# Optimization experiments

Measured on AMD Instinct MI355X. Metric: run time of the kernel, lower is better.

## Reference

```python
import jax, jax.numpy as jnp
import numpy as np

EPSILON = 0.0014  # ODIN perturbation magnitude (init kwarg)


def _penultimate(x, W, b):
    # Simple feature extractor standing in for model.penultimate_forward:
    # flatten image and apply ReLU(linear). feat: [B, D]
    B = x.shape[0]
    return jax.nn.relu(x.reshape(B, -1) @ W + b)


def _mahalanobis_scores(feat, mu, invsig):
    # diff: [B, C, D]; y[b,c] = -diff[b,c] @ invsig @ diff[b,c]
    # Fused as a single einsum instead of the naive [B,C,D,D] broadcast.
    diff = feat[:, None, :] - mu[None, :, :]
    return -jnp.einsum('bcd,de,bce->bc', diff, invsig, diff)


def setup_inputs() -> dict:
    key = jax.random.key(0)
    k1, k2, k3, k4, k5 = jax.random.split(key, 5)
    B, C, D, IN = 1024, 100, 512, 3 * 32 * 32
    x = jax.random.uniform(k1, (B, 3, 32, 32), dtype=jnp.float32)
    W = jax.random.normal(k2, (IN, D), dtype=jnp.float32) * (1.0 / np.sqrt(IN))
    b = jax.random.normal(k3, (D,), dtype=jnp.float32) * 0.01
    mu = jax.random.normal(k4, (C, D), dtype=jnp.float32)
    # symmetric positive-definite inverse covariance
    A = jax.random.normal(k5, (D, D), dtype=jnp.float32) * (1.0 / np.sqrt(D))
    invsig = A @ A.T + jnp.eye(D, dtype=jnp.float32)
    return {"x": x, "W": W, "b": b, "mu": mu, "invsig": invsig}


def reference(x, W, b, mu, invsig):
    # FGSM step: perturb x toward increasing the max class score.
    def fgsm_loss(xx):
        y = _mahalanobis_scores(_penultimate(xx, W, b), mu, invsig)
        return jnp.max(y, axis=1).sum()

    g = jax.grad(fgsm_loss)(x)
    # torch.autograd.grad(create_graph=False) detaches the grad -> stop_gradient
    x_adv = jnp.clip(x + EPSILON * jax.lax.stop_gradient(g), 0.0, 1.0)
    # Main pass on the perturbed input.
    return _mahalanobis_scores(_penultimate(x_adv, W, b), mu, invsig)
```

## Files before the change

kernel.cpp:

```cpp
#include <hip/hip_runtime.h>
#include <hip/hip_bf16.h>

#define EPS_ODIN 0.0014f

constexpr int Bb  = 1024;
constexpr int Cc  = 100;
constexpr int Dd  = 512;
constexpr int INn = 3072;
constexpr int PITCH = 68;

using s16x8 = __attribute__((ext_vector_type(8))) short;
using s16x4 = __attribute__((ext_vector_type(4))) short;
using f32x4 = __attribute__((ext_vector_type(4))) float;

__device__ __forceinline__ short f2bf(float f) {
    __hip_bfloat16 h = __float2bfloat16(f);
    return *reinterpret_cast<short*>(&h);
}

__global__ __launch_bounds__(256) void prep_kernel(
    const float* __restrict__ x, const float* __restrict__ W,
    const float* __restrict__ invsig, const float* __restrict__ mu,
    short* __restrict__ x_b, short* __restrict__ Wt_b,
    short* __restrict__ is_b, short* __restrict__ mu_b)
{
    __shared__ float tp[32][33];
    const int tid = threadIdx.x, bid = blockIdx.x;
    const long gstride = (long)gridDim.x * 256;
    auto cvt4 = [&](const float* in, short* ob, long q) {
        long idx = q * 4;
        f32x4 v = *(const f32x4*)(in + idx);
        s16x4 o;
        #pragma unroll
        for (int j = 0; j < 4; ++j) o[j] = f2bf(v[j]);
        *(s16x4*)(ob + idx) = o;
    };
    for (long i = (long)bid * 256 + tid; i < (long)Bb * INn / 4; i += gstride) cvt4(x, x_b, i);
    for (long i = (long)bid * 256 + tid; i < (long)Dd * Dd / 4; i += gstride) cvt4(invsig, is_b, i);
    for (long i = (long)bid * 256 + tid; i < (long)112 * Dd / 4; i += gstride) {
        long idx = i * 4;
        if ((idx >> 9) < Cc) cvt4(mu, mu_b, i);
        else *(s16x4*)(mu_b + idx) = s16x4{0, 0, 0, 0};
    }

    const int tx = tid & 31, ty = tid >> 5;
    for (int tix = bid; tix < (INn / 32) * (Dd / 32); tix += gridDim.x) {
        int r0 = (tix >> 4) * 32, c0 = (tix & 15) * 32;
        #pragma unroll
        for (int i2 = 0; i2 < 4; ++i2)
            tp[ty + i2 * 8][tx] = W[(long)(r0 + ty + i2 * 8) * Dd + c0 + tx];
        __syncthreads();
        #pragma unroll
        for (int i2 = 0; i2 < 4; ++i2) {
            int c = c0 + ty + i2 * 8;
            Wt_b[(long)c * INn + r0 + tx] = f2bf(tp[tx][ty + i2 * 8]);
        }
        __syncthreads();
    }
}

__global__ __launch_bounds__(256) void im_q_kernel(
    const float* __restrict__ mu, const float* __restrict__ invsig,
    float* __restrict__ im, float* __restrict__ q)
{
    __shared__ float muc[512];
    __shared__ float red[4];
    const int tid = threadIdx.x, c = blockIdx.x;
    for (int e = tid; e < 512; e += 256) muc[e] = mu[(long)c * 512 + e];
    __syncthreads();
    const int d0 = tid, d1 = tid + 256;
    float a0 = 0.f, a1 = 0.f, a2 = 0.f, a3 = 0.f;
    for (int e = 0; e < 512; e += 2) {
        float m0 = muc[e], m1 = muc[e + 1];
        a0 = fmaf(m0, invsig[(long)e * 512 + d0], a0);
        a1 = fmaf(m0, invsig[(long)e * 512 + d1], a1);
        a2 = fmaf(m1, invsig[(long)(e + 1) * 512 + d0], a2);
        a3 = fmaf(m1, invsig[(long)(e + 1) * 512 + d1], a3);
    }
    float r0 = a0 + a2, r1 = a1 + a3;
    im[(long)c * 512 + d0] = r0;
    im[(long)c * 512 + d1] = r1;
    float s = muc[d0] * r0 + muc[d1] * r1;
    #pragma unroll
    for (int off = 32; off; off >>= 1) s += __shfl_down(s, off);
    if ((tid & 63) == 0) red[tid >> 6] = s;
    __syncthreads();
    if (tid == 0) q[c] = red[0] + red[1] + red[2] + red[3];
}

template<int EPI>
__global__ __launch_bounds__(256, 4) void gemm_b1(
    const short* __restrict__ A, const short* __restrict__ Bm,
    float* __restrict__ Cm, long K, int kcount, int N, long sstr,
    const float* __restrict__ aux1, const float* __restrict__ aux2,
    short* __restrict__ obf, float esc)
{
    __shared__ short As[128 * PITCH];
    __shared__ short Bs[64 * PITCH];
    const int tid = threadIdx.x;
    const int m0 = blockIdx.y * 128, n0 = blockIdx.x * 64;
    const long kbeg = (long)blockIdx.z * kcount;
    const int lane = tid & 63, w = tid >> 6, wm = w * 32;
    const int lrow = lane & 15, kseg = lane >> 4;
    const int srow = tid >> 3, skc = (tid & 7) * 8;
    const int nkt = kcount >> 6;

    f32x4 acc[2][4];
    #pragma unroll
    for (int i = 0; i < 2; ++i)
        #pragma unroll
        for (int j = 0; j < 4; ++j)
            acc[i][j] = f32x4{0.f, 0.f, 0.f, 0.f};

    s16x8 rA[4], rB[2];
    auto ldA = [&](int kt) {
        #pragma unroll
        for (int i = 0; i < 4; ++i)
            rA[i] = *(const s16x8*)(A + (long)(m0 + srow + i * 32) * K + kbeg + (long)kt * 64 + skc);
    };
    auto ldB = [&](int kt) {
        #pragma unroll
        for (int i = 0; i < 2; ++i)
            rB[i] = *(const s16x8*)(Bm + (long)(n0 + srow + i * 32) * K + kbeg + (long)kt * 64 + skc);
    };

    ldA(0); ldB(0);
    for (int kt = 0; kt < nkt; ++kt) {
        #pragma unroll
        for (int i = 0; i < 4; ++i)
            *(s16x8*)&As[(srow + i * 32) * PITCH + skc] = rA[i];
        #pragma unroll
        for (int i = 0; i < 2; ++i)
            *(s16x8*)&Bs[(srow + i * 32) * PITCH + skc] = rB[i];
        __syncthreads();
        if (kt + 1 < nkt) { ldA(kt + 1); ldB(kt + 1); }
        #pragma unroll
        for (int kk = 0; kk < 2; ++kk) {
            s16x8 ah[2], bfr[4];
            #pragma unroll
            for (int i = 0; i < 2; ++i)
                ah[i] = *(const s16x8*)&As[(wm + i * 16 + lrow) * PITCH + kk * 32 + kseg * 8];
            #pragma unroll
            for (int j = 0; j < 4; ++j)
                bfr[j] = *(const s16x8*)&Bs[(j * 16 + lrow) * PITCH + kk * 32 + kseg * 8];
            #pragma unroll
            for (int i = 0; i < 2; ++i)
                #pragma unroll
                for (int j = 0; j < 4; ++j)
                    acc[i][j] = __builtin_amdgcn_mfma_f32_16x16x32_bf16(ah[i], bfr[j], acc[i][j], 0, 0, 0);
        }
        __syncthreads();
    }

    const int crow = (lane >> 4) * 4, ccol = lane & 15;
    #pragma unroll
    for (int i = 0; i < 2; ++i)
        #pragma unroll
        for (int j = 0; j < 4; ++j)
            #pragma unroll
            for (int r = 0; r < 4; ++r) {
                int gm = m0 + wm + i * 16 + crow + r;
                int gn = n0 + j * 16 + ccol;
                float v = acc[i][j][r];
                if (EPI == 0) {
                    (Cm + (long)blockIdx.z * sstr)[(long)gm * 512 + gn] = v;
                } else if (EPI == 1) {
                    long cidx = (long)gm * N + gn;
                    Cm[cidx] = v;
                    obf[cidx] = f2bf(v);
                } else {
                    long cidx = (long)gm * N + gn;
                    float u = fmaxf(aux1[cidx] + aux2[gn] + esc * v, 0.f);
                    Cm[cidx] = u;
                    obf[cidx] = f2bf(u);
                }
            }
}

__global__ __launch_bounds__(256) void reduce_feat(
    const float* __restrict__ part, const float* __restrict__ bias,
    float* __restrict__ featpre, float* __restrict__ feat, short* __restrict__ fb)
{
    long idx = ((long)blockIdx.x * 256 + threadIdx.x) * 4;
    f32x4 v = *(const f32x4*)(part + idx);
    #pragma unroll
    for (int z = 1; z < 8; ++z)
        v += *(const f32x4*)(part + (long)z * Bb * Dd + idx);
    *(f32x4*)(featpre + idx) = v;
    f32x4 bb = *(const f32x4*)(bias + (idx & 511));
    s16x4 o;
    #pragma unroll
    for (int j = 0; j < 4; ++j) {
        v[j] = fmaxf(v[j] + bb[j], 0.f);
        o[j] = f2bf(v[j]);
    }
    *(f32x4*)(feat + idx) = v;
    *(s16x4*)(fb + idx) = o;
}

__global__ __launch_bounds__(256) void reduce_wtw(
    const float* __restrict__ wpart, short* __restrict__ wtw_b)
{
    long idx = ((long)blockIdx.x * 256 + threadIdx.x) * 4;
    f32x4 v = *(const f32x4*)(wpart + idx);
    #pragma unroll
    for (int z = 1; z < 8; ++z)
        v += *(const f32x4*)(wpart + (long)z * Dd * Dd + idx);
    s16x4 o;
    #pragma unroll
    for (int j = 0; j < 4; ++j) o[j] = f2bf(v[j]);
    *(s16x4*)(wtw_b + idx) = o;
}

__global__ __launch_bounds__(256) void tail_a(
    const short* __restrict__ h_b, const short* __restrict__ mu_b,
    const float* __restrict__ feat, const float* __restrict__ hbuf,
    const float* __restrict__ im, const float* __restrict__ q,
    short* __restrict__ dz_b)
{
    __shared__ f32x4 red[4][7][64];
    __shared__ int cstv[16];
    const int tid = threadIdx.x, lane = tid & 63, w = tid >> 6;
    const int m0 = blockIdx.x * 16;
    const int arow = lane & 15, kseg = lane >> 4;

    f32x4 acc[7];
    #pragma unroll
    for (int j = 0; j < 7; ++j) acc[j] = f32x4{0.f, 0.f, 0.f, 0.f};

    const long abase = (long)(m0 + arow) * 512 + w * 128 + kseg * 8;
    const long bbase = (long)arow * 512 + w * 128 + kseg * 8;
    #pragma unroll
    for (int kt = 0; kt < 4; ++kt) {
        s16x8 av = *(const s16x8*)(h_b + abase + kt * 32);
        #pragma unroll
        for (int j = 0; j < 7; ++j) {
            s16x8 bv = *(const s16x8*)(mu_b + bbase + (long)j * 16 * 512 + kt * 32);
            acc[j] = __builtin_amdgcn_mfma_f32_16x16x32_bf16(av, bv, acc[j], 0, 0, 0);
        }
    }
    #pragma unroll
    for (int j = 0; j < 7; ++j) red[w][j][lane] = acc[j];
    __syncthreads();

    if (w == 0) {
        #pragma unroll
        for (int j = 0; j < 7; ++j) {
            f32x4 s0 = red[0][j][lane];
            #pragma unroll
            for (int ww = 1; ww < 4; ++ww) s0 += red[ww][j][lane];
            acc[j] = s0;
        }
        const int crow = (lane >> 4) * 4, ccol = lane & 15;
        #pragma unroll
        for (int r = 0; r < 4; ++r) {
            float best = -INFINITY; int bestc = 0;
            #pragma unroll
            for (int j = 0; j < 7; ++j) {
                int n = j * 16 + ccol;
                if (n < 100) {
                    float v = 2.f * acc[j][r] - q[n];
                    if (v > best) { best = v; bestc = n; }
                }
            }
            #pragma unroll
            for (int mk = 1; mk <= 8; mk <<= 1) {
                float ov = __shfl_xor(best, mk);
                int   oc = __shfl_xor(bestc, mk);
                if (ov > best || (ov == best && oc < bestc)) { best = ov; bestc = oc; }
            }
            if (ccol == 0) cstv[crow + r] = bestc;
        }
    }
    __syncthreads();

    #pragma unroll
    for (int it = 0; it < 8; ++it) {
        int i4 = it * 256 + tid;
        int r = i4 >> 7, d4 = (i4 & 127) * 4;
        long gi = (long)(m0 + r) * 512 + d4;
        f32x4 fv = *(const f32x4*)(feat + gi);
        f32x4 hv = *(const f32x4*)(hbuf + gi);
        f32x4 iv = *(const f32x4*)(im + (long)cstv[r] * 512 + d4);
        s16x4 o;
        #pragma unroll
        for (int jj = 0; jj < 4; ++jj) {
            float v = (fv[jj] > 0.f) ? -2.f * (hv[jj] - iv[jj]) : 0.f;
            o[jj] = f2bf(v);
        }
        *(s16x4*)(dz_b + gi) = o;
    }
}

__global__ __launch_bounds__(256) void tail_b(
    const short* __restrict__ h_b, const short* __restrict__ mu_b,
    const float* __restrict__ feat, const float* __restrict__ hbuf,
    const float* __restrict__ q, float* __restrict__ out)
{
    __shared__ f32x4 red[4][7][64];
    __shared__ float srow[16];
    const int tid = threadIdx.x, lane = tid & 63, w = tid >> 6;
    const int m0 = blockIdx.x * 16;
    const int arow = lane & 15, kseg = lane >> 4;

    #pragma unroll
    for (int rr = 0; rr < 4; ++rr) {
        int r = w * 4 + rr;
        long gi = (long)(m0 + r) * 512 + lane * 8;
        f32x4 a0 = *(const f32x4*)(feat + gi);
        f32x4 a1 = *(const f32x4*)(feat + gi + 4);
        f32x4 b0 = *(const f32x4*)(hbuf + gi);
        f32x4 b1 = *(const f32x4*)(hbuf + gi + 4);
        float ss = 0.f;
        #pragma unroll
        for (int jj = 0; jj < 4; ++jj) ss += a0[jj] * b0[jj] + a1[jj] * b1[jj];
        #pragma unroll
        for (int off = 32; off; off >>= 1) ss += __shfl_down(ss, off);
        if (lane == 0) srow[r] = ss;
    }

    f32x4 acc[7];
    #pragma unroll
    for (int j = 0; j < 7; ++j) acc[j] = f32x4{0.f, 0.f, 0.f, 0.f};
    const long abase = (long)(m0 + arow) * 512 + w * 128 + kseg * 8;
    const long bbase = (long)arow * 512 + w * 128 + kseg * 8;
    #pragma unroll
    for (int kt = 0; kt < 4; ++kt) {
        s16x8 av = *(const s16x8*)(h_b + abase + kt * 32);
        #pragma unroll
        for (int j = 0; j < 7; ++j) {
            s16x8 bv = *(const s16x8*)(mu_b + bbase + (long)j * 16 * 512 + kt * 32);
            acc[j] = __builtin_amdgcn_mfma_f32_16x16x32_bf16(av, bv, acc[j], 0, 0, 0);
        }
    }
    #pragma unroll
    for (int j = 0; j < 7; ++j) red[w][j][lane] = acc[j];
    __syncthreads();

    if (w == 0) {
        const int crow = (lane >> 4) * 4, ccol = lane & 15;
        #pragma unroll
        for (int j = 0; j < 7; ++j) {
            int n = j * 16 + ccol;
            if (n >= 100) continue;
            f32x4 s0 = red[0][j][lane];
            #pragma unroll
            for (int ww = 1; ww < 4; ++ww) s0 += red[ww][j][lane];
            float qn = q[n];
            #pragma unroll
            for (int r = 0; r < 4; ++r)
                out[(long)(m0 + crow + r) * 100 + n] = 2.f * s0[r] - srow[crow + r] - qn;
        }
    }
}

extern "C" void kernel_launch(void* const* d_in, const int* in_sizes, int n_in,
                              void* d_out, int out_size, void* d_ws, size_t ws_size,
                              hipStream_t stream)
{
    const float* x      = (const float*)d_in[0];
    const float* W      = (const float*)d_in[1];
    const float* bias   = (const float*)d_in[2];
    const float* mu     = (const float*)d_in[3];
    const float* invsig = (const float*)d_in[4];
    float* out = (float*)d_out;

    char* wp = (char*)d_ws;
    auto alloc = [&](size_t bytes) { char* p = wp; wp += (bytes + 255) & ~size_t(255); return p; };
    short* x_b   = (short*)alloc((size_t)Bb * INn * 2);
    short* Wt_b  = (short*)alloc((size_t)Dd * INn * 2);
    short* is_b  = (short*)alloc((size_t)Dd * Dd * 2);
    short* mu_b  = (short*)alloc((size_t)112 * Dd * 2);
    short* wtw_b = (short*)alloc((size_t)Dd * Dd * 2);
    float* im    = (float*)alloc((size_t)Cc * Dd * 4);
    float* q     = (float*)alloc(512);
    float* part  = (float*)alloc((size_t)8 * Bb * Dd * 4);
    float* wpart = (float*)alloc((size_t)8 * Dd * Dd * 4);
    float* featpre = (float*)alloc((size_t)Bb * Dd * 4);
    float* feat  = (float*)alloc((size_t)Bb * Dd * 4);
    short* f_b   = (short*)alloc((size_t)Bb * Dd * 2);
    float* hbuf  = (float*)alloc((size_t)Bb * Dd * 4);
    short* h_b   = (short*)alloc((size_t)Bb * Dd * 2);
    short* dz_b  = (short*)alloc((size_t)Bb * Dd * 2);

    dim3 blk(256);

    prep_kernel<<<512, blk, 0, stream>>>(x, W, invsig, mu, x_b, Wt_b, is_b, mu_b);
    im_q_kernel<<<Cc, blk, 0, stream>>>(mu, invsig, im, q);
    gemm_b1<0><<<dim3(8, 4, 8), blk, 0, stream>>>(
        Wt_b, Wt_b, wpart, INn, INn / 8, Dd, (long)Dd * Dd, nullptr, nullptr, nullptr, 0.f);
    reduce_wtw<<<256, blk, 0, stream>>>(wpart, wtw_b);
    gemm_b1<0><<<dim3(8, 8, 8), blk, 0, stream>>>(
        x_b, Wt_b, part, INn, INn / 8, Dd, (long)Bb * Dd, nullptr, nullptr, nullptr, 0.f);
    reduce_feat<<<512, blk, 0, stream>>>(part, bias, featpre, feat, f_b);
    gemm_b1<1><<<dim3(8, 8), blk, 0, stream>>>(
        f_b, is_b, hbuf, Dd, Dd, Dd, 0, nullptr, nullptr, h_b, 0.f);
    tail_a<<<Bb / 16, blk, 0, stream>>>(h_b, mu_b, feat, hbuf, im, q, dz_b);
    gemm_b1<3><<<dim3(8, 8), blk, 0, stream>>>(
        dz_b, wtw_b, feat, Dd, Dd, Dd, 0, featpre, bias, f_b, EPS_ODIN);
    gemm_b1<1><<<dim3(8, 8), blk, 0, stream>>>(
        f_b, is_b, hbuf, Dd, Dd, Dd, 0, nullptr, nullptr, h_b, 0.f);
    tail_b<<<Bb / 16, blk, 0, stream>>>(h_b, mu_b, feat, hbuf, q, out);
}
```

Before: 108.8 us.

## Convert x to bf16 inside GEMM, exploit WtW symmetry, use smaller square-GEMM tiles

Removes the separate fp32-to-bf16 pass over x by loading fp32 x directly in the feature GEMM and converting while staging into shared memory. The W^T W Gram GEMM now computes only upper-triangular block tiles (20 instead of 32) and mirrors each result into the transposed position. The three 512x512-K GEMMs move to a new 64x64-tile kernel with twice as many blocks, to raise occupancy across the many compute units. In exchange, the A loads in the main GEMM read twice as many bytes from global memory, and the mirrored writes in the Gram kernel are uncoalesced.

```diff
diff --git a/kernel.cpp b/kernel.cpp
--- a/kernel.cpp
+++ b/kernel.cpp
@@ -19,10 +19,8 @@
 }
 
 __global__ __launch_bounds__(256) void prep_kernel(
-    const float* __restrict__ x, const float* __restrict__ W,
-    const float* __restrict__ invsig, const float* __restrict__ mu,
-    short* __restrict__ x_b, short* __restrict__ Wt_b,
-    short* __restrict__ is_b, short* __restrict__ mu_b)
+    const float* __restrict__ W, const float* __restrict__ invsig, const float* __restrict__ mu,
+    short* __restrict__ Wt_b, short* __restrict__ is_b, short* __restrict__ mu_b)
 {
     __shared__ float tp[32][33];
     const int tid = threadIdx.x, bid = blockIdx.x;
@@ -35,14 +33,12 @@
         for (int j = 0; j < 4; ++j) o[j] = f2bf(v[j]);
         *(s16x4*)(ob + idx) = o;
     };
-    for (long i = (long)bid * 256 + tid; i < (long)Bb * INn / 4; i += gstride) cvt4(x, x_b, i);
     for (long i = (long)bid * 256 + tid; i < (long)Dd * Dd / 4; i += gstride) cvt4(invsig, is_b, i);
     for (long i = (long)bid * 256 + tid; i < (long)112 * Dd / 4; i += gstride) {
         long idx = i * 4;
         if ((idx >> 9) < Cc) cvt4(mu, mu_b, i);
         else *(s16x4*)(mu_b + idx) = s16x4{0, 0, 0, 0};
     }
-
     const int tx = tid & 31, ty = tid >> 5;
     for (int tix = bid; tix < (INn / 32) * (Dd / 32); tix += gridDim.x) {
         int r0 = (tix >> 4) * 32, c0 = (tix & 15) * 32;
@@ -88,15 +84,15 @@
     if (tid == 0) q[c] = red[0] + red[1] + red[2] + red[3];
 }
 
-template<int EPI>
-__global__ __launch_bounds__(256, 4) void gemm_b1(
-    const short* __restrict__ A, const short* __restrict__ Bm,
-    float* __restrict__ Cm, long K, int kcount, int N, long sstr,
-    const float* __restrict__ aux1, const float* __restrict__ aux2,
-    short* __restrict__ obf, float esc)
+template<bool AF32>
+__global__ __launch_bounds__(256, 4) void gemm_part(
+    const void* __restrict__ Av, const short* __restrict__ Bm,
+    float* __restrict__ Cm, long K, int kcount, long sstr)
 {
     __shared__ short As[128 * PITCH];
     __shared__ short Bs[64 * PITCH];
+    const short* A  = (const short*)Av;
+    const float* Af = (const float*)Av;
     const int tid = threadIdx.x;
     const int m0 = blockIdx.y * 128, n0 = blockIdx.x * 64;
     const long kbeg = (long)blockIdx.z * kcount;
@@ -113,10 +109,14 @@
             acc[i][j] = f32x4{0.f, 0.f, 0.f, 0.f};
 
     s16x8 rA[4], rB[2];
+    f32x4 rAf[4][2];
     auto ldA = [&](int kt) {
         #pragma unroll
-        for (int i = 0; i < 4; ++i)
-            rA[i] = *(const s16x8*)(A + (long)(m0 + srow + i * 32) * K + kbeg + (long)kt * 64 + skc);
+        for (int i = 0; i < 4; ++i) {
+            long off = (long)(m0 + srow + i * 32) * K + kbeg + (long)kt * 64 + skc;
+            if (AF32) { rAf[i][0] = *(const f32x4*)(Af + off); rAf[i][1] = *(const f32x4*)(Af + off + 4); }
+            else      { rA[i] = *(const s16x8*)(A + off); }
+        }
     };
     auto ldB = [&](int kt) {
         #pragma unroll
@@ -127,8 +127,16 @@
     ldA(0); ldB(0);
     for (int kt = 0; kt < nkt; ++kt) {
         #pragma unroll
-        for (int i = 0; i < 4; ++i)
-            *(s16x8*)&As[(srow + i * 32) * PITCH + skc] = rA[i];
+        for (int i = 0; i < 4; ++i) {
+            if (AF32) {
+                s16x8 o;
+                #pragma unroll
+                for (int j = 0; j < 4; ++j) { o[j] = f2bf(rAf[i][0][j]); o[4 + j] = f2bf(rAf[i][1][j]); }
+                *(s16x8*)&As[(srow + i * 32) * PITCH + skc] = o;
+            } else {
+                *(s16x8*)&As[(srow + i * 32) * PITCH + skc] = rA[i];
+            }
+        }
         #pragma unroll
         for (int i = 0; i < 2; ++i)
             *(s16x8*)&Bs[(srow + i * 32) * PITCH + skc] = rB[i];
@@ -153,6 +161,82 @@
     }
 
     const int crow = (lane >> 4) * 4, ccol = lane & 15;
+    float* dst = Cm + (long)blockIdx.z * sstr;
+    #pragma unroll
+    for (int i = 0; i < 2; ++i)
+        #pragma unroll
+        for (int j = 0; j < 4; ++j)
+            #pragma unroll
+            for (int r = 0; r < 4; ++r)
+                dst[(long)(m0 + wm + i * 16 + crow + r) * 512 + n0 + j * 16 + ccol] = acc[i][j][r];
+}
+
+__global__ __launch_bounds__(256, 4) void wtw_part(
+    const short* __restrict__ Wt_b, float* __restrict__ wpart)
+{
+    __shared__ short As[128 * PITCH];
+    __shared__ short Bs[64 * PITCH];
+    const int tid = threadIdx.x;
+    int t = blockIdx.x, tm, tn;
+    if (t < 8)       { tm = 0; tn = t; }
+    else if (t < 14) { tm = 1; tn = t - 6; }
+    else if (t < 18) { tm = 2; tn = t - 10; }
+    else             { tm = 3; tn = t - 12; }
+    const int m0 = tm * 128, n0 = tn * 64;
+    const long kbeg = (long)blockIdx.y * 384;
+    const int lane = tid & 63, w = tid >> 6, wm = w * 32;
+    const int lrow = lane & 15, kseg = lane >> 4;
+    const int srow = tid >> 3, skc = (tid & 7) * 8;
+
+    f32x4 acc[2][4];
+    #pragma unroll
+    for (int i = 0; i < 2; ++i)
+        #pragma unroll
+        for (int j = 0; j < 4; ++j)
+            acc[i][j] = f32x4{0.f, 0.f, 0.f, 0.f};
+
+    s16x8 rA[4], rB[2];
+    auto ldA = [&](int kt) {
+        #pragma unroll
+        for (int i = 0; i < 4; ++i)
+            rA[i] = *(const s16x8*)(Wt_b + (long)(m0 + srow + i * 32) * INn + kbeg + (long)kt * 64 + skc);
+    };
+    auto ldB = [&](int kt) {
+        #pragma unroll
+        for (int i = 0; i < 2; ++i)
+            rB[i] = *(const s16x8*)(Wt_b + (long)(n0 + srow + i * 32) * INn + kbeg + (long)kt * 64 + skc);
+    };
+
+    ldA(0); ldB(0);
+    for (int kt = 0; kt < 6; ++kt) {
+        #pragma unroll
+        for (int i = 0; i < 4; ++i)
+            *(s16x8*)&As[(srow + i * 32) * PITCH + skc] = rA[i];
+        #pragma unroll
+        for (int i = 0; i < 2; ++i)
+            *(s16x8*)&Bs[(srow + i * 32) * PITCH + skc] = rB[i];
+        __syncthreads();
+        if (kt + 1 < 6) { ldA(kt + 1); ldB(kt + 1); }
+        #pragma unroll
+        for (int kk = 0; kk < 2; ++kk) {
+            s16x8 ah[2], bfr[4];
+            #pragma unroll
+            for (int i = 0; i < 2; ++i)
+                ah[i] = *(const s16x8*)&As[(wm + i * 16 + lrow) * PITCH + kk * 32 + kseg * 8];
+            #pragma unroll
+            for (int j = 0; j < 4; ++j)
+                bfr[j] = *(const s16x8*)&Bs[(j * 16 + lrow) * PITCH + kk * 32 + kseg * 8];
+            #pragma unroll
+            for (int i = 0; i < 2; ++i)
+                #pragma unroll
+                for (int j = 0; j < 4; ++j)
+                    acc[i][j] = __builtin_amdgcn_mfma_f32_16x16x32_bf16(ah[i], bfr[j], acc[i][j], 0, 0, 0);
+        }
+        __syncthreads();
+    }
+
+    const int crow = (lane >> 4) * 4, ccol = lane & 15;
+    float* dst = wpart + (long)blockIdx.y * Dd * Dd;
     #pragma unroll
     for (int i = 0; i < 2; ++i)
         #pragma unroll
@@ -162,18 +246,8 @@
                 int gm = m0 + wm + i * 16 + crow + r;
                 int gn = n0 + j * 16 + ccol;
                 float v = acc[i][j][r];
-                if (EPI == 0) {
-                    (Cm + (long)blockIdx.z * sstr)[(long)gm * 512 + gn] = v;
-                } else if (EPI == 1) {
-                    long cidx = (long)gm * N + gn;
-                    Cm[cidx] = v;
-                    obf[cidx] = f2bf(v);
-                } else {
-                    long cidx = (long)gm * N + gn;
-                    float u = fmaxf(aux1[cidx] + aux2[gn] + esc * v, 0.f);
-                    Cm[cidx] = u;
-                    obf[cidx] = f2bf(u);
-                }
+                dst[(long)gm * 512 + gn] = v;
+                dst[(long)gn * 512 + gm] = v;
             }
 }
 
@@ -210,6 +284,73 @@
     #pragma unroll
     for (int j = 0; j < 4; ++j) o[j] = f2bf(v[j]);
     *(s16x4*)(wtw_b + idx) = o;
+}
+
+template<int EPI>
+__global__ __launch_bounds__(256, 4) void gemm_sq(
+    const short* __restrict__ A, const short* __restrict__ Bm,
+    float* __restrict__ Cm,
+    const float* __restrict__ aux1, const float* __restrict__ aux2,
+    short* __restrict__ obf, float esc)
+{
+    __shared__ short As[64 * PITCH];
+    __shared__ short Bs[64 * PITCH];
+    const int tid = threadIdx.x;
+    const int m0 = blockIdx.y * 64, n0 = blockIdx.x * 64;
+    const int lane = tid & 63, w = tid >> 6;
+    const int lrow = lane & 15, kseg = lane >> 4;
+    const int srow = tid >> 2, skc = (tid & 3) * 16;
+
+    f32x4 acc[4];
+    #pragma unroll
+    for (int j = 0; j < 4; ++j) acc[j] = f32x4{0.f, 0.f, 0.f, 0.f};
+
+    s16x8 rA[2], rB[2];
+    auto ld = [&](int kt) {
+        long ao = (long)(m0 + srow) * 512 + kt * 64 + skc;
+        long bo = (long)(n0 + srow) * 512 + kt * 64 + skc;
+        rA[0] = *(const s16x8*)(A + ao);  rA[1] = *(const s16x8*)(A + ao + 8);
+        rB[0] = *(const s16x8*)(Bm + bo); rB[1] = *(const s16x8*)(Bm + bo + 8);
+    };
+
+    ld(0);
+    for (int kt = 0; kt < 8; ++kt) {
+        *(s16x8*)&As[srow * PITCH + skc]     = rA[0];
+        *(s16x8*)&As[srow * PITCH + skc + 8] = rA[1];
+        *(s16x8*)&Bs[srow * PITCH + skc]     = rB[0];
+        *(s16x8*)&Bs[srow * PITCH + skc + 8] = rB[1];
+        __syncthreads();
+        if (kt + 1 < 8) ld(kt + 1);
+        #pragma unroll
+        for (int kk = 0; kk < 2; ++kk) {
+            s16x8 av = *(const s16x8*)&As[(w * 16 + lrow) * PITCH + kk * 32 + kseg * 8];
+            #pragma unroll
+            for (int j = 0; j < 4; ++j) {
+                s16x8 bv = *(const s16x8*)&Bs[(j * 16 + lrow) * PITCH + kk * 32 + kseg * 8];
+                acc[j] = __builtin_amdgcn_mfma_f32_16x16x32_bf16(av, bv, acc[j], 0, 0, 0);
+            }
+        }
+        __syncthreads();
+    }
+
+    const int crow = (lane >> 4) * 4, ccol = lane & 15;
+    #pragma unroll
+    for (int j = 0; j < 4; ++j)
+        #pragma unroll
+        for (int r = 0; r < 4; ++r) {
+            int gm = m0 + w * 16 + crow + r;
+            int gn = n0 + j * 16 + ccol;
+            long cidx = (long)gm * 512 + gn;
+            float v = acc[j][r];
+            if (EPI == 1) {
+                Cm[cidx] = v;
+                obf[cidx] = f2bf(v);
+            } else {
+                float u = fmaxf(aux1[cidx] + aux2[gn] + esc * v, 0.f);
+                Cm[cidx] = u;
+                obf[cidx] = f2bf(u);
+            }
+        }
 }
 
 __global__ __launch_bounds__(256) void tail_a(
@@ -367,7 +508,6 @@
 
     char* wp = (char*)d_ws;
     auto alloc = [&](size_t bytes) { char* p = wp; wp += (bytes + 255) & ~size_t(255); return p; };
-    short* x_b   = (short*)alloc((size_t)Bb * INn * 2);
     short* Wt_b  = (short*)alloc((size_t)Dd * INn * 2);
     short* is_b  = (short*)alloc((size_t)Dd * Dd * 2);
     short* mu_b  = (short*)alloc((size_t)112 * Dd * 2);
@@ -385,20 +525,16 @@
 
     dim3 blk(256);
 
-    prep_kernel<<<512, blk, 0, stream>>>(x, W, invsig, mu, x_b, Wt_b, is_b, mu_b);
+    prep_kernel<<<256, blk, 0, stream>>>(W, invsig, mu, Wt_b, is_b, mu_b);
     im_q_kernel<<<Cc, blk, 0, stream>>>(mu, invsig, im, q);
-    gemm_b1<0><<<dim3(8, 4, 8), blk, 0, stream>>>(
-        Wt_b, Wt_b, wpart, INn, INn / 8, Dd, (long)Dd * Dd, nullptr, nullptr, nullptr, 0.f);
+    wtw_part<<<dim3(20, 8), blk, 0, stream>>>(Wt_b, wpart);
     reduce_wtw<<<256, blk, 0, stream>>>(wpart, wtw_b);
-    gemm_b1<0><<<dim3(8, 8, 8), blk, 0, stream>>>(
-        x_b, Wt_b, part, INn, INn / 8, Dd, (long)Bb * Dd, nullptr, nullptr, nullptr, 0.f);
+    gemm_part<true><<<dim3(8, 8, 8), blk, 0, stream>>>(
+        (const void*)x, Wt_b, part, INn, INn / 8, (long)Bb * Dd);
     reduce_feat<<<512, blk, 0, stream>>>(part, bias, featpre, feat, f_b);
-    gemm_b1<1><<<dim3(8, 8), blk, 0, stream>>>(
-        f_b, is_b, hbuf, Dd, Dd, Dd, 0, nullptr, nullptr, h_b, 0.f);
+    gemm_sq<1><<<dim3(8, 16), blk, 0, stream>>>(f_b, is_b, hbuf, nullptr, nullptr, h_b, 0.f);
     tail_a<<<Bb / 16, blk, 0, stream>>>(h_b, mu_b, feat, hbuf, im, q, dz_b);
-    gemm_b1<3><<<dim3(8, 8), blk, 0, stream>>>(
-        dz_b, wtw_b, feat, Dd, Dd, Dd, 0, featpre, bias, f_b, EPS_ODIN);
-    gemm_b1<1><<<dim3(8, 8), blk, 0, stream>>>(
-        f_b, is_b, hbuf, Dd, Dd, Dd, 0, nullptr, nullptr, h_b, 0.f);
+    gemm_sq<3><<<dim3(8, 16), blk, 0, stream>>>(dz_b, wtw_b, feat, featpre, bias, f_b, EPS_ODIN);
+    gemm_sq<1><<<dim3(8, 16), blk, 0, stream>>>(f_b, is_b, hbuf, nullptr, nullptr, h_b, 0.f);
     tail_b<<<Bb / 16, blk, 0, stream>>>(h_b, mu_b, feat, hbuf, q, out);
 }
```

New measurement: 115.1 us. 1.06x slower.
